# Performance work log

Hardware: AMD Instinct MI355X
Metric: run time of the kernel (lower is better)

The kernel has to match this reference:

```python
import jax, jax.numpy as jnp
import numpy as np

NUM_FEATURE = 512
HIDDEN = 256
NUM_CLASSES = 10
L1 = 1e-4
ALPHA = 1e-3
BATCH = 65536


def setup_inputs() -> dict:
    key = jax.random.key(0)
    k = jax.random.split(key, 6)
    x = jax.random.normal(k[0], (BATCH, NUM_FEATURE), dtype=jnp.float32)
    y = jax.random.randint(k[1], (BATCH,), 0, NUM_CLASSES, dtype=jnp.int32)
    fc0 = jax.random.normal(k[2], (NUM_FEATURE, 512), dtype=jnp.float32) / NUM_FEATURE
    fc1 = jax.random.normal(k[3], (NUM_FEATURE, 512), dtype=jnp.float32) / NUM_FEATURE
    w = jax.random.normal(k[4], (NUM_FEATURE, HIDDEN), dtype=jnp.float32) / NUM_FEATURE
    w1 = jax.random.normal(k[5], (HIDDEN, NUM_CLASSES), dtype=jnp.float32) / HIDDEN
    return {"x": x, "y": y, "fc0": fc0, "fc1": fc1, "w": w, "w1": w1}


def reference(x, y, fc0, fc1, w, w1):
    # sigmoid-gated MLP block with residual
    x1 = x @ fc0                                   # [B, 512]
    x2 = jax.nn.relu(x @ fc1)                      # [B, 512]
    x4 = x + (1.0 + jax.nn.sigmoid(x1)) * x2       # [B, 512] residual

    # head (Dropout(p=0.0) is identity)
    logits = jax.nn.relu(x4 @ w) @ w1              # [B, 10]
    pred = jnp.argmax(logits, axis=1)

    # cross-entropy (mean over batch)
    logp = jax.nn.log_softmax(logits, axis=-1)
    ce = -jnp.mean(jnp.take_along_axis(logp, y[:, None].astype(jnp.int32), axis=1))

    # L1 penalty on all weight matrices
    l1_pen = L1 * (jnp.abs(w1).sum() + jnp.abs(w).sum()
                   + jnp.abs(fc0).sum() + jnp.abs(fc1).sum())

    # per-class variance: sum_i ||mean_{y_i} - x4_i||^2, vectorized via segment sums
    counts = jax.ops.segment_sum(jnp.ones((x4.shape[0],), jnp.float32), y,
                                 num_segments=NUM_CLASSES)
    sums = jax.ops.segment_sum(x4, y, num_segments=NUM_CLASSES)   # [10, 512]
    means = sums / jnp.maximum(counts, 1.0)[:, None]
    var_loss = jnp.sum(jnp.square(means[y] - x4))

    loss = ce + l1_pen + ALPHA * var_loss
    acc = jnp.mean((pred.astype(jnp.int32) == y.astype(jnp.int32)).astype(jnp.float32))
    return (loss, acc)
```

## Files before the change

kernel.cpp:

```cpp
#include <hip/hip_runtime.h>
#include <stdint.h>

#define BATCH 65536
#define FDIM 512
#define HDIM 256
#define NC 10
#define NREP 16

typedef short short8 __attribute__((ext_vector_type(8)));
typedef float f32x4 __attribute__((ext_vector_type(4)));

#define OFF_FC0T   ((size_t)0)
#define OFF_FC1T   (OFF_FC0T + (size_t)512*512*2)
#define OFF_WT     (OFF_FC1T + (size_t)512*512*2)
#define OFF_XT     (OFF_WT   + (size_t)256*512*2)
#define OFF_X4T    (OFF_XT   + (size_t)BATCH*512*2)
#define OFF_ACC    (OFF_X4T  + (size_t)BATCH*512*2)
#define SCAL_SUMSQ 0
#define SCAL_CE    16
#define SCAL_ACC   32
#define SCAL_L1    48
#define SCAL_CTR   64
#define SCAL_N     128
#define CNT_OFF    SCAL_N
#define GSUM_OFF   (SCAL_N + NREP*16)
#define ACC_FLOATS (GSUM_OFF + NREP*5120)
#define OFF_W1T    (OFF_ACC + (size_t)ACC_FLOATS*4)

#define GLL(g,l) __builtin_amdgcn_global_load_lds((const __attribute__((address_space(1))) void*)(g), (__attribute__((address_space(3))) void*)(l), 16, 0, 0)

__device__ __forceinline__ unsigned short f2b(float f){
  unsigned u = __float_as_uint(f);
  u += 0x7FFFu + ((u >> 16) & 1u);
  return (unsigned short)(u >> 16);
}
__device__ __forceinline__ float b2f(unsigned short h){
  return __uint_as_float(((unsigned)h) << 16);
}
__device__ __forceinline__ unsigned pk2b(float f0, float f1){
  unsigned u0 = __float_as_uint(f0) + 0x8000u;
  unsigned u1 = __float_as_uint(f1) + 0x8000u;
  return __builtin_amdgcn_perm(u1, u0, 0x07060302u);
}
__device__ __forceinline__ float ald(const float* p){
  return __hip_atomic_load(p, __ATOMIC_RELAXED, __HIP_MEMORY_SCOPE_AGENT);
}

__global__ __launch_bounds__(256) void k_setup(
    const float* __restrict__ x,   const float* __restrict__ fc0,
    const float* __restrict__ fc1, const float* __restrict__ w,
    const float* __restrict__ w1,  const int* __restrict__ y,
    unsigned short* __restrict__ xT,   unsigned short* __restrict__ fc0T,
    unsigned short* __restrict__ fc1T, unsigned short* __restrict__ wT,
    unsigned short* __restrict__ w1T,  float* __restrict__ accb)
{
  int blk = blockIdx.x, t = threadIdx.x;
  if (blk < 2048){
    __shared__ __align__(16) unsigned short xls[16*520];
    int wv = t >> 6, l = t & 63;
    #pragma unroll 1
    for (int it = 0; it < 2; ++it){
      int I = blk*2 + it;
      #pragma unroll
      for (int rr = 0; rr < 4; ++rr){
        int row = wv*4 + rr;
        const float* src = x + ((size_t)(I*16 + row))*FDIM + l*8;
        float4 v0 = *(const float4*)src;
        float4 v1 = *(const float4*)(src + 4);
        unsigned o[4];
        o[0] = pk2b(v0.x, v0.y); o[1] = pk2b(v0.z, v0.w);
        o[2] = pk2b(v1.x, v1.y); o[3] = pk2b(v1.z, v1.w);
        *(short8*)&xls[row*520 + l*8] = *(short8*)o;
      }
      __syncthreads();
      #pragma unroll
      for (int cc = 0; cc < 4; ++cc){
        int C = cc*4 + wv;
        short8 v = *(const short8*)&xls[(l & 15)*520 + C*32 + (l >> 4)*8];
        *(short8*)&xT[(((size_t)I*16 + C) << 9) + l*8] = v;
      }
      __syncthreads();
    }
    return;
  }
  if (blk < 2384){
    int i = (blk - 2048)*256 + t;
    float l1v = 0.f;
    if (i < 32768){
      int n4 = i&15, m = (i>>4)&3, C = (i>>6)&15, J = i>>10;
      int n = J*16+n4, k8 = C*4+m;
      unsigned short o[8];
      #pragma unroll
      for (int j=0;j<8;++j){ float v = fc0[(size_t)(k8*8+j)*512 + n]; o[j]=f2b(v); l1v += fabsf(v); }
      *(short8*)&fc0T[(size_t)(J*16+C)*512 + (i&63)*8] = *(short8*)o;
    } else if (i < 65536){
      int j0 = i - 32768;
      int n4 = j0&15, m = (j0>>4)&3, C = (j0>>6)&15, J = j0>>10;
      int n = J*16+n4, k8 = C*4+m;
      unsigned short o[8];
      #pragma unroll
      for (int j=0;j<8;++j){ float v = fc1[(size_t)(k8*8+j)*512 + n]; o[j]=f2b(v); l1v += fabsf(v); }
      *(short8*)&fc1T[(size_t)(J*16+C)*512 + (j0&63)*8] = *(short8*)o;
    } else if (i < 81920){
      int j0 = i - 65536;
      int n4 = j0&15, m = (j0>>4)&3, C = (j0>>6)&15, J = j0>>10;
      int n = J*16+n4, k8 = C*4+m;
      unsigned short o[8];
      #pragma unroll
      for (int j=0;j<8;++j){ float v = w[(size_t)(k8*8+j)*256 + n]; o[j]=f2b(v); l1v += fabsf(v); }
      *(short8*)&wT[(size_t)(J*16+C)*512 + (j0&63)*8] = *(short8*)o;
    } else if (i < 86016){
      int j0 = i - 81920;
      int C = j0 >> 9, l = (j0 >> 3) & 63, e = j0 & 7;
      int n = l & 15, k = C*32 + (l>>4)*8 + e;
      float v = (n < NC) ? w1[k*NC + n] : 0.f;
      w1T[C*512 + l*8 + e] = f2b(v);
      if (n < NC) l1v = fabsf(v);
    }
    for (int off = 32; off; off >>= 1) l1v += __shfl_down(l1v, off);
    if ((t & 63) == 0 && l1v != 0.f)
      atomicAdd(&accb[SCAL_L1 + (blk & (NREP-1))], l1v);
    return;
  }
  if (blk < 2465){
    int base = (blk - 2384)*1024;
    #pragma unroll
    for (int j=0;j<4;++j){
      int idx = base + j*256 + t;
      if (idx < ACC_FLOATS && (idx < CNT_OFF || idx >= CNT_OFF + NREP*16))
        accb[idx] = 0.f;
    }
    return;
  }
  {
    __shared__ float cntS[16];
    int b = blk - 2465;
    if (t < 16) cntS[t] = 0.f;
    __syncthreads();
    int base = b*4096;
    for (int i = t; i < 4096; i += 256) atomicAdd(&cntS[y[base+i]], 1.f);
    __syncthreads();
    if (t < 16) accb[CNT_OFF + b*16 + t] = cntS[t];
  }
}


#define BARRIER() __builtin_amdgcn_s_barrier()
#define LGKM0() do{ asm volatile("s_waitcnt lgkmcnt(0)" ::: "memory"); \
                    __builtin_amdgcn_sched_barrier(0); }while(0)

#define RA(AB, C) do{                                                         \
  _Pragma("unroll") for (int m_=0;m_<8;++m_)                                  \
    a[m_] = *(const short8*)((AB) + (((wr*8+m_)*2 + (C))<<10) + lane*16);     \
}while(0)

#define RB(AB, MAT, C) do{                                                    \
  _Pragma("unroll") for (int n_=0;n_<2;++n_)                                  \
    bb[n_] = *(const short8*)((AB) + 32768 + (MAT)*16384 +                    \
                              (((wc*2+n_)*2 + (C))<<10) + lane*16);           \
}while(0)

#define MM16(ACC) do{                                                         \
  __builtin_amdgcn_s_setprio(1);                                              \
  _Pragma("unroll") for (int n_=0;n_<2;++n_)                                  \
  _Pragma("unroll") for (int m_=0;m_<8;++m_)                                  \
    ACC[m_][n_] = __builtin_amdgcn_mfma_f32_16x16x32_bf16(a[m_], bb[n_], ACC[m_][n_], 0,0,0); \
  __builtin_amdgcn_s_setprio(0);                                              \
}while(0)

#define SA(KT, C) do{                                                         \
  char* d_ = ldsd + (((KT)&1) ? 65536 : 0);                                   \
  _Pragma("unroll") for (int r_=0;r_<2;++r_){                                 \
    int I_ = wv + r_*8;                                                       \
    GLL(xb + (((size_t)((rowblk*16 + I_)*16 + (KT)*2 + (C))) << 10) + lane*16,\
        d_ + ((I_*2 + (C)) << 10) + lane*16);                                 \
  } }while(0)

#define SB(KT, C) do{                                                         \
  char* d_ = ldsd + (((KT)&1) ? 65536 : 0) + 32768;                           \
  GLL(b0b + (((size_t)((colblk*8 + wv)*16 + (KT)*2 + (C))) << 10) + lane*16,  \
      d_ + ((wv*2 + (C)) << 10) + lane*16);                                   \
  GLL(b1b + (((size_t)((colblk*8 + wv)*16 + (KT)*2 + (C))) << 10) + lane*16,  \
      d_ + 16384 + ((wv*2 + (C)) << 10) + lane*16);                           \
}while(0)

#define KLOOP() do{                                                           \
  SA(0,0); SB(0,0); SA(0,1); SB(0,1); SA(1,0); SB(1,0); SA(1,1);              \
  asm volatile("s_waitcnt vmcnt(6)" ::: "memory");                            \
  __builtin_amdgcn_sched_barrier(0);                                          \
  BARRIER();                                                                  \
  _Pragma("unroll")                                                           \
  for (int i = 0; i < 4; ++i){                                                \
    int kt0 = 2*i, kt1 = 2*i+1;                                               \
    char* Ab0 = ldsd + ((kt0 & 1) ? 65536 : 0);                               \
    char* Ab1 = ldsd + ((kt1 & 1) ? 65536 : 0);                               \
    RA(Ab0, 0); RB(Ab0, 0, 0);                                                \
    SB(kt1, 1);                                                               \
    BARRIER(); LGKM0(); MM16(acc1);                                           \
    BARRIER();                                                                \
    RB(Ab0, 1, 0);                                                            \
    if (i < 3) SA(kt0+2, 0);                                                  \
    BARRIER(); LGKM0(); MM16(acc2);                                           \
    BARRIER();                                                                \
    RA(Ab0, 1); RB(Ab0, 0, 1);                                                \
    if (i < 3) SB(kt0+2, 0);                                                  \
    BARRIER(); LGKM0(); MM16(acc1);                                           \
    BARRIER();                                                                \
    RB(Ab0, 1, 1);                                                            \
    if (i < 3) SA(kt0+2, 1);                                                  \
    BARRIER(); LGKM0(); MM16(acc2);                                           \
    if (i < 3) { asm volatile("s_waitcnt vmcnt(6)" ::: "memory"); }           \
    else       { asm volatile("s_waitcnt vmcnt(0)" ::: "memory"); }           \
    __builtin_amdgcn_sched_barrier(0);                                        \
    BARRIER();                                                                \
    RA(Ab1, 0); RB(Ab1, 0, 0);                                                \
    if (i < 3) SB(kt0+2, 1);                                                  \
    BARRIER(); LGKM0(); MM16(acc1);                                           \
    BARRIER();                                                                \
    RB(Ab1, 1, 0);                                                            \
    if (i < 3) SA(kt1+2, 0);                                                  \
    BARRIER(); LGKM0(); MM16(acc2);                                           \
    BARRIER();                                                                \
    RA(Ab1, 1); RB(Ab1, 0, 1);                                                \
    if (i < 3) SB(kt1+2, 0);                                                  \
    BARRIER(); LGKM0(); MM16(acc1);                                           \
    BARRIER();                                                                \
    RB(Ab1, 1, 1);                                                            \
    if (i < 3) SA(kt1+2, 1);                                                  \
    BARRIER(); LGKM0(); MM16(acc2);                                           \
    if (i < 3) { asm volatile("s_waitcnt vmcnt(6)" ::: "memory");             \
                 __builtin_amdgcn_sched_barrier(0); }                         \
    BARRIER();                                                                \
  }                                                                           \
}while(0)

__global__ __launch_bounds__(512, 2) void k_gemm12(
    const unsigned short* __restrict__ xT,
    const unsigned short* __restrict__ fc0T,
    const unsigned short* __restrict__ fc1T,
    const int* __restrict__ y,
    unsigned short* __restrict__ x4T,
    float* __restrict__ accb)
{
  extern __shared__ __align__(16) char ldsd[];
  float* scal = accb;
  float* gsum = accb + GSUM_OFF;

  int blk = blockIdx.x;
  int wg = (blk & 7)*128 + (blk >> 3);
  int rowblk = wg >> 2;
  int colblk = wg & 3;

  int t = threadIdx.x;
  int wv = t >> 6, lane = t & 63, ln = lane & 15, quad = lane >> 4;
  int wr = wv >> 2, wc = wv & 3;

  const char* xb  = (const char*)xT;
  const char* b0b = (const char*)fc0T;
  const char* b1b = (const char*)fc1T;

  const f32x4 zv = {0.f,0.f,0.f,0.f};
  f32x4 acc1[8][2], acc2[8][2];
  #pragma unroll
  for (int m=0;m<8;++m){ acc1[m][0]=zv; acc1[m][1]=zv; acc2[m][0]=zv; acc2[m][1]=zv; }

  short8 a[8], bb[2];

  KLOOP();

  {
    int Cres = colblk*4 + wc;
    #pragma unroll
    for (int i = 0; i < 8; ++i){
      GLL(xb + (((size_t)((rowblk*16 + wr*8 + i)*16 + Cres)) << 10) + lane*16,
          ldsd + ((wv*8 + i) << 10) + lane*16);
    }
    asm volatile("s_waitcnt vmcnt(0)" ::: "memory");
  }
  __syncthreads();

  unsigned short* resU = (unsigned short*)ldsd;
  unsigned short* x4U  = (unsigned short*)(ldsd + 65536);
  float sumsq = 0.f;
  #pragma unroll
  for (int m = 0; m < 8; ++m){
    #pragma unroll
    for (int n = 0; n < 2; ++n){
      #pragma unroll
      for (int r = 0; r < 4; ++r){
        int slot = (quad*4 + r) | ((n*2 + (ln>>3)) << 4);
        int idx = ((wv*8 + m) << 9) + slot*8 + (ln & 7);
        float xv  = b2f(resU[idx]);
        float x1v = acc1[m][n][r];
        float x2v = fmaxf(acc2[m][n][r], 0.f);
        float gate = 1.f + 1.f/(1.f + __expf(-x1v));
        float x4v = fmaf(gate, x2v, xv);
        unsigned short ub = f2b(x4v);
        float fq = b2f(ub);
        sumsq = fmaf(fq, fq, sumsq);
        x4U[idx] = ub;
        acc1[m][n][r] = fq;
      }
    }
  }
  for (int off = 32; off; off >>= 1) sumsq += __shfl_down(sumsq, off);
  __syncthreads();

  float cs[NC][2];
  #pragma unroll
  for (int c=0;c<NC;++c){ cs[c][0]=0.f; cs[c][1]=0.f; }
  {
    const int* yrow = y + rowblk*256 + wr*128;
    #pragma unroll
    for (int m = 0; m < 8; ++m){
      int yv[4];
      #pragma unroll
      for (int r = 0; r < 4; ++r) yv[r] = yrow[m*16 + quad*4 + r];
      #pragma unroll
      for (int r = 0; r < 4; ++r){
        float v0 = acc1[m][0][r], v1 = acc1[m][1][r];
        #pragma unroll
        for (int c = 0; c < NC; ++c){
          bool msk = (yv[r] == c);
          cs[c][0] += msk ? v0 : 0.f;
          cs[c][1] += msk ? v1 : 0.f;
        }
      }
    }
  }
  #pragma unroll
  for (int c = 0; c < NC; ++c)
    #pragma unroll
    for (int n = 0; n < 2; ++n){
      cs[c][n] += __shfl_xor(cs[c][n], 16);
      cs[c][n] += __shfl_xor(cs[c][n], 32);
    }

  float* red = (float*)ldsd;
  float* ct  = (float*)(ldsd + 4096);
  if (lane == 0) red[wv] = sumsq;
  if (lane < 16){
    #pragma unroll
    for (int c = 0; c < NC; ++c)
      #pragma unroll
      for (int n = 0; n < 2; ++n)
        ct[((wv*NC + c)*2 + n)*16 + ln] = cs[c][n];
  }
  __syncthreads();
  if (t == 0){
    float s = 0.f;
    #pragma unroll
    for (int i=0;i<8;++i) s += red[i];
    atomicAdd(&scal[SCAL_SUMSQ + (blk & (NREP-1))], s);
  }
  #pragma unroll
  for (int r = 0; r < 2; ++r){
    int o = r*512 + t;
    int tile = o >> 6, off16 = o & 63;
    int wvp = tile >> 3, i = tile & 7;
    size_t Ig = (size_t)rowblk*16 + (wvp>>2)*8 + i;
    int Cg = colblk*4 + (wvp & 3);
    *(short8*)&x4T[((Ig*16 + Cg) << 9) + off16*8] =
      *(const short8*)&x4U[(tile << 9) + off16*8];
  }
  for (int i = t; i < NC*128; i += 512){
    int c = i >> 7, col = i & 127;
    int wcx = col >> 5, nx = (col >> 4) & 1, lnx = col & 15;
    float v = ct[((wcx*NC + c)*2 + nx)*16 + lnx]
            + ct[(((4+wcx)*NC + c)*2 + nx)*16 + lnx];
    atomicAdd(&gsum[(size_t)(blk & (NREP-1))*5120 + c*512 + colblk*128 + col], v);
  }
}

__global__ __launch_bounds__(512, 2) void k_gemm3_head(
    const unsigned short* __restrict__ x4T,
    const unsigned short* __restrict__ wT,
    const unsigned short* __restrict__ w1T,
    const int* __restrict__ y,
    float* __restrict__ accb,
    float* __restrict__ out)
{
  extern __shared__ __align__(16) char ldsd[];
  __shared__ float redc[8], reda[8];
  __shared__ int lastB;

  float* scal = accb;

  int blk = blockIdx.x;
  int rowblk = blk;
  const int colblk = 0;

  int t = threadIdx.x;
  int wv = t >> 6, lane = t & 63, ln = lane & 15, quad = lane >> 4;
  int wr = wv >> 2, wc = wv & 3;
  int rep = (blk ^ (blk >> 4)) & (NREP-1);

  const char* xb  = (const char*)x4T;
  const char* b0b = (const char*)wT;
  const char* b1b = (const char*)wT + (size_t)128*1024;

  const f32x4 zv = {0.f,0.f,0.f,0.f};
  f32x4 acc1[8][2], acc2[8][2];
  #pragma unroll
  for (int m=0;m<8;++m){ acc1[m][0]=zv; acc1[m][1]=zv; acc2[m][0]=zv; acc2[m][1]=zv; }

  short8 a[8], bb[2];

  KLOOP();

  short8 bw1[8];
  #pragma unroll
  for (int Ck = 0; Ck < 8; ++Ck)
    bw1[Ck] = *(const short8*)&w1T[Ck*512 + lane*8];

  unsigned short* transH = (unsigned short*)ldsd;
  #pragma unroll
  for (int m = 0; m < 8; ++m){
    #pragma unroll
    for (int n = 0; n < 2; ++n){
      #pragma unroll
      for (int r = 0; r < 4; ++r){
        int slot = (quad*4 + r) | ((n*2 + (ln>>3)) << 4);
        int e = ln & 7;
        int IhA = wr*8 + m;
        transH[((IhA*8 + wc)     << 9) + slot*8 + e] = f2b(fmaxf(acc1[m][n][r], 0.f));
        transH[((IhA*8 + 4 + wc) << 9) + slot*8 + e] = f2b(fmaxf(acc2[m][n][r], 0.f));
      }
    }
  }
  __syncthreads();

  f32x4 alog[2] = {zv, zv};
  #pragma unroll
  for (int ih = 0; ih < 2; ++ih){
    int Ih = wv*2 + ih;
    #pragma unroll
    for (int Ck = 0; Ck < 8; ++Ck){
      short8 af = *(const short8*)&transH[((Ih*8 + Ck) << 9) + lane*8];
      alog[ih] = __builtin_amdgcn_mfma_f32_16x16x32_bf16(af, bw1[Ck], alog[ih], 0,0,0);
    }
  }

  float ce_l = 0.f, acc_l = 0.f;
  #pragma unroll
  for (int ih = 0; ih < 2; ++ih){
    #pragma unroll
    for (int r = 0; r < 4; ++r){
      int grow = blk*256 + (wv*2 + ih)*16 + quad*4 + r;
      int yv = y[grow];
      float lg = (ln < NC) ? alog[ih][r] : -1e30f;
      float m = lg; int mi = ln;
      #pragma unroll
      for (int mk = 1; mk < 16; mk <<= 1){
        float om = __shfl_xor(m, mk); int oi = __shfl_xor(mi, mk);
        if (om > m || (om == m && oi < mi)){ m = om; mi = oi; }
      }
      float e  = (ln < NC) ? __expf(lg - m) : 0.f;
      float sy = (ln == yv) ? lg : 0.f;
      #pragma unroll
      for (int mk = 1; mk < 16; mk <<= 1){ e += __shfl_xor(e, mk); sy += __shfl_xor(sy, mk); }
      float lse = m + __logf(e);
      if (ln == 0){ ce_l += (lse - sy); acc_l += (mi == yv) ? 1.f : 0.f; }
    }
  }
  ce_l  += __shfl_down(ce_l, 16);  acc_l += __shfl_down(acc_l, 16);
  ce_l  += __shfl_down(ce_l, 32);  acc_l += __shfl_down(acc_l, 32);
  if (lane == 0){ redc[wv] = ce_l; reda[wv] = acc_l; }
  __syncthreads();
  if (t == 0){
    float c = 0.f, aa = 0.f;
    #pragma unroll
    for (int i=0;i<8;++i){ c += redc[i]; aa += reda[i]; }
    atomicAdd(&scal[SCAL_CE  + rep], c);
    atomicAdd(&scal[SCAL_ACC + rep], aa);
    __threadfence();
    int prev = atomicAdd((int*)(scal + SCAL_CTR), 1);
    lastB = (prev == (int)gridDim.x - 1);
  }
  __syncthreads();
  if (!lastB) return;

  {
    const float* gsum = accb + GSUM_OFF;
    const float* gcnt = accb + CNT_OFF;
    float contrib = 0.f;
    for (int idx = t; idx < 5120; idx += 512){
      float S = 0.f;
      #pragma unroll
      for (int r = 0; r < NREP; ++r) S += ald(&gsum[(size_t)r*5120 + idx]);
      int c = idx >> 9;
      float cnt = 0.f;
      #pragma unroll
      for (int r = 0; r < NREP; ++r) cnt += ald(&gcnt[r*16 + c]);
      contrib += S*S / fmaxf(cnt, 1.f);
    }
    for (int off = 32; off; off >>= 1) contrib += __shfl_down(contrib, off);
    __syncthreads();
    if (lane == 0) redc[wv] = contrib;
    __syncthreads();
    if (t == 0){
      float var2 = 0.f;
      #pragma unroll
      for (int i=0;i<8;++i) var2 += redc[i];
      float sumsq=0.f, ce=0.f, accv=0.f, l1=0.f;
      for (int r=0;r<NREP;++r){
        sumsq += ald(&scal[SCAL_SUMSQ+r]);
        ce    += ald(&scal[SCAL_CE+r]);
        accv  += ald(&scal[SCAL_ACC+r]);
        l1    += ald(&scal[SCAL_L1+r]);
      }
      float var_loss = sumsq - var2;
      out[0] = ce/(float)BATCH + 1e-4f*l1 + 1e-3f*var_loss;
      out[1] = accv/(float)BATCH;
    }
  }
}

extern "C" void kernel_launch(void* const* d_in, const int* in_sizes, int n_in,
                              void* d_out, int out_size, void* d_ws, size_t ws_size,
                              hipStream_t stream){
  (void)in_sizes; (void)n_in; (void)out_size; (void)ws_size;
  const float* x   = (const float*)d_in[0];
  const int*   y   = (const int*)d_in[1];
  const float* fc0 = (const float*)d_in[2];
  const float* fc1 = (const float*)d_in[3];
  const float* w   = (const float*)d_in[4];
  const float* w1  = (const float*)d_in[5];
  char* ws = (char*)d_ws;
  unsigned short* fc0T = (unsigned short*)(ws + OFF_FC0T);
  unsigned short* fc1T = (unsigned short*)(ws + OFF_FC1T);
  unsigned short* wT   = (unsigned short*)(ws + OFF_WT);
  unsigned short* xT   = (unsigned short*)(ws + OFF_XT);
  unsigned short* x4T  = (unsigned short*)(ws + OFF_X4T);
  unsigned short* w1T  = (unsigned short*)(ws + OFF_W1T);
  float* accb = (float*)(ws + OFF_ACC);

  static bool once = [](){
    hipFuncSetAttribute((const void*)k_gemm12,
                        hipFuncAttributeMaxDynamicSharedMemorySize, 131072);
    hipFuncSetAttribute((const void*)k_gemm3_head,
                        hipFuncAttributeMaxDynamicSharedMemorySize, 131072);
    return true;
  }();
  (void)once;

  k_setup<<<2481, 256, 0, stream>>>(x, fc0, fc1, w, w1, y, xT, fc0T, fc1T, wT, w1T, accb);
  k_gemm12<<<1024, 512, 131072, stream>>>(xT, fc0T, fc1T, y, x4T, accb);
  k_gemm3_head<<<256, 512, 131072, stream>>>(x4T, wT, w1T, y, accb, (float*)d_out);
}
```

Before: 354.8 us.

## Fuse setup and both GEMM stages into one persistent cooperative kernel

Replaces the three launches (setup, gemm12, gemm3+head) with one cooperative kernel of 256 blocks that uses grid.sync between phases. Each block now loops over four column tiles of the first GEMM instead of using 1024 separate blocks, and y labels are staged in LDS. The aim is to remove launch gaps and the last-block atomic counter. In exchange, occupancy drops to one 512-thread block per CU, 256 blocks cover 256 CUs, and grid-wide barriers add their own cost.

```diff
diff --git a/kernel.cpp b/kernel.cpp
--- a/kernel.cpp
+++ b/kernel.cpp
@@ -1,5 +1,8 @@
 #include <hip/hip_runtime.h>
+#include <hip/hip_cooperative_groups.h>
 #include <stdint.h>
+
+namespace cg = cooperative_groups;
 
 #define BATCH 65536
 #define FDIM 512
@@ -20,7 +23,6 @@
 #define SCAL_CE    16
 #define SCAL_ACC   32
 #define SCAL_L1    48
-#define SCAL_CTR   64
 #define SCAL_N     128
 #define CNT_OFF    SCAL_N
 #define GSUM_OFF   (SCAL_N + NREP*16)
@@ -46,104 +48,6 @@
   return __hip_atomic_load(p, __ATOMIC_RELAXED, __HIP_MEMORY_SCOPE_AGENT);
 }
 
-__global__ __launch_bounds__(256) void k_setup(
-    const float* __restrict__ x,   const float* __restrict__ fc0,
-    const float* __restrict__ fc1, const float* __restrict__ w,
-    const float* __restrict__ w1,  const int* __restrict__ y,
-    unsigned short* __restrict__ xT,   unsigned short* __restrict__ fc0T,
-    unsigned short* __restrict__ fc1T, unsigned short* __restrict__ wT,
-    unsigned short* __restrict__ w1T,  float* __restrict__ accb)
-{
-  int blk = blockIdx.x, t = threadIdx.x;
-  if (blk < 2048){
-    __shared__ __align__(16) unsigned short xls[16*520];
-    int wv = t >> 6, l = t & 63;
-    #pragma unroll 1
-    for (int it = 0; it < 2; ++it){
-      int I = blk*2 + it;
-      #pragma unroll
-      for (int rr = 0; rr < 4; ++rr){
-        int row = wv*4 + rr;
-        const float* src = x + ((size_t)(I*16 + row))*FDIM + l*8;
-        float4 v0 = *(const float4*)src;
-        float4 v1 = *(const float4*)(src + 4);
-        unsigned o[4];
-        o[0] = pk2b(v0.x, v0.y); o[1] = pk2b(v0.z, v0.w);
-        o[2] = pk2b(v1.x, v1.y); o[3] = pk2b(v1.z, v1.w);
-        *(short8*)&xls[row*520 + l*8] = *(short8*)o;
-      }
-      __syncthreads();
-      #pragma unroll
-      for (int cc = 0; cc < 4; ++cc){
-        int C = cc*4 + wv;
-        short8 v = *(const short8*)&xls[(l & 15)*520 + C*32 + (l >> 4)*8];
-        *(short8*)&xT[(((size_t)I*16 + C) << 9) + l*8] = v;
-      }
-      __syncthreads();
-    }
-    return;
-  }
-  if (blk < 2384){
-    int i = (blk - 2048)*256 + t;
-    float l1v = 0.f;
-    if (i < 32768){
-      int n4 = i&15, m = (i>>4)&3, C = (i>>6)&15, J = i>>10;
-      int n = J*16+n4, k8 = C*4+m;
-      unsigned short o[8];
-      #pragma unroll
-      for (int j=0;j<8;++j){ float v = fc0[(size_t)(k8*8+j)*512 + n]; o[j]=f2b(v); l1v += fabsf(v); }
-      *(short8*)&fc0T[(size_t)(J*16+C)*512 + (i&63)*8] = *(short8*)o;
-    } else if (i < 65536){
-      int j0 = i - 32768;
-      int n4 = j0&15, m = (j0>>4)&3, C = (j0>>6)&15, J = j0>>10;
-      int n = J*16+n4, k8 = C*4+m;
-      unsigned short o[8];
-      #pragma unroll
-      for (int j=0;j<8;++j){ float v = fc1[(size_t)(k8*8+j)*512 + n]; o[j]=f2b(v); l1v += fabsf(v); }
-      *(short8*)&fc1T[(size_t)(J*16+C)*512 + (j0&63)*8] = *(short8*)o;
-    } else if (i < 81920){
-      int j0 = i - 65536;
-      int n4 = j0&15, m = (j0>>4)&3, C = (j0>>6)&15, J = j0>>10;
-      int n = J*16+n4, k8 = C*4+m;
-      unsigned short o[8];
-      #pragma unroll
-      for (int j=0;j<8;++j){ float v = w[(size_t)(k8*8+j)*256 + n]; o[j]=f2b(v); l1v += fabsf(v); }
-      *(short8*)&wT[(size_t)(J*16+C)*512 + (j0&63)*8] = *(short8*)o;
-    } else if (i < 86016){
-      int j0 = i - 81920;
-      int C = j0 >> 9, l = (j0 >> 3) & 63, e = j0 & 7;
-      int n = l & 15, k = C*32 + (l>>4)*8 + e;
-      float v = (n < NC) ? w1[k*NC + n] : 0.f;
-      w1T[C*512 + l*8 + e] = f2b(v);
-      if (n < NC) l1v = fabsf(v);
-    }
-    for (int off = 32; off; off >>= 1) l1v += __shfl_down(l1v, off);
-    if ((t & 63) == 0 && l1v != 0.f)
-      atomicAdd(&accb[SCAL_L1 + (blk & (NREP-1))], l1v);
-    return;
-  }
-  if (blk < 2465){
-    int base = (blk - 2384)*1024;
-    #pragma unroll
-    for (int j=0;j<4;++j){
-      int idx = base + j*256 + t;
-      if (idx < ACC_FLOATS && (idx < CNT_OFF || idx >= CNT_OFF + NREP*16))
-        accb[idx] = 0.f;
-    }
-    return;
-  }
-  {
-    __shared__ float cntS[16];
-    int b = blk - 2465;
-    if (t < 16) cntS[t] = 0.f;
-    __syncthreads();
-    int base = b*4096;
-    for (int i = t; i < 4096; i += 256) atomicAdd(&cntS[y[base+i]], 1.f);
-    __syncthreads();
-    if (t < 16) accb[CNT_OFF + b*16 + t] = cntS[t];
-  }
-}
-
 
 #define BARRIER() __builtin_amdgcn_s_barrier()
 #define LGKM0() do{ asm volatile("s_waitcnt lgkmcnt(0)" ::: "memory"); \
@@ -234,254 +138,318 @@
   }                                                                           \
 }while(0)
 
-__global__ __launch_bounds__(512, 2) void k_gemm12(
-    const unsigned short* __restrict__ xT,
-    const unsigned short* __restrict__ fc0T,
-    const unsigned short* __restrict__ fc1T,
-    const int* __restrict__ y,
-    unsigned short* __restrict__ x4T,
-    float* __restrict__ accb)
-{
-  extern __shared__ __align__(16) char ldsd[];
-  float* scal = accb;
-  float* gsum = accb + GSUM_OFF;
-
-  int blk = blockIdx.x;
-  int wg = (blk & 7)*128 + (blk >> 3);
-  int rowblk = wg >> 2;
-  int colblk = wg & 3;
-
-  int t = threadIdx.x;
-  int wv = t >> 6, lane = t & 63, ln = lane & 15, quad = lane >> 4;
-  int wr = wv >> 2, wc = wv & 3;
-
-  const char* xb  = (const char*)xT;
-  const char* b0b = (const char*)fc0T;
-  const char* b1b = (const char*)fc1T;
-
-  const f32x4 zv = {0.f,0.f,0.f,0.f};
-  f32x4 acc1[8][2], acc2[8][2];
-  #pragma unroll
-  for (int m=0;m<8;++m){ acc1[m][0]=zv; acc1[m][1]=zv; acc2[m][0]=zv; acc2[m][1]=zv; }
-
-  short8 a[8], bb[2];
-
-  KLOOP();
-
-  {
-    int Cres = colblk*4 + wc;
-    #pragma unroll
-    for (int i = 0; i < 8; ++i){
-      GLL(xb + (((size_t)((rowblk*16 + wr*8 + i)*16 + Cres)) << 10) + lane*16,
-          ldsd + ((wv*8 + i) << 10) + lane*16);
-    }
-    asm volatile("s_waitcnt vmcnt(0)" ::: "memory");
-  }
-  __syncthreads();
-
-  unsigned short* resU = (unsigned short*)ldsd;
-  unsigned short* x4U  = (unsigned short*)(ldsd + 65536);
-  float sumsq = 0.f;
-  #pragma unroll
-  for (int m = 0; m < 8; ++m){
-    #pragma unroll
-    for (int n = 0; n < 2; ++n){
-      #pragma unroll
-      for (int r = 0; r < 4; ++r){
-        int slot = (quad*4 + r) | ((n*2 + (ln>>3)) << 4);
-        int idx = ((wv*8 + m) << 9) + slot*8 + (ln & 7);
-        float xv  = b2f(resU[idx]);
-        float x1v = acc1[m][n][r];
-        float x2v = fmaxf(acc2[m][n][r], 0.f);
-        float gate = 1.f + 1.f/(1.f + __expf(-x1v));
-        float x4v = fmaf(gate, x2v, xv);
-        unsigned short ub = f2b(x4v);
-        float fq = b2f(ub);
-        sumsq = fmaf(fq, fq, sumsq);
-        x4U[idx] = ub;
-        acc1[m][n][r] = fq;
-      }
-    }
-  }
-  for (int off = 32; off; off >>= 1) sumsq += __shfl_down(sumsq, off);
-  __syncthreads();
-
-  float cs[NC][2];
-  #pragma unroll
-  for (int c=0;c<NC;++c){ cs[c][0]=0.f; cs[c][1]=0.f; }
-  {
-    const int* yrow = y + rowblk*256 + wr*128;
-    #pragma unroll
-    for (int m = 0; m < 8; ++m){
-      int yv[4];
-      #pragma unroll
-      for (int r = 0; r < 4; ++r) yv[r] = yrow[m*16 + quad*4 + r];
-      #pragma unroll
-      for (int r = 0; r < 4; ++r){
-        float v0 = acc1[m][0][r], v1 = acc1[m][1][r];
-        #pragma unroll
-        for (int c = 0; c < NC; ++c){
-          bool msk = (yv[r] == c);
-          cs[c][0] += msk ? v0 : 0.f;
-          cs[c][1] += msk ? v1 : 0.f;
-        }
-      }
-    }
-  }
-  #pragma unroll
-  for (int c = 0; c < NC; ++c)
-    #pragma unroll
-    for (int n = 0; n < 2; ++n){
-      cs[c][n] += __shfl_xor(cs[c][n], 16);
-      cs[c][n] += __shfl_xor(cs[c][n], 32);
-    }
-
-  float* red = (float*)ldsd;
-  float* ct  = (float*)(ldsd + 4096);
-  if (lane == 0) red[wv] = sumsq;
-  if (lane < 16){
-    #pragma unroll
-    for (int c = 0; c < NC; ++c)
-      #pragma unroll
-      for (int n = 0; n < 2; ++n)
-        ct[((wv*NC + c)*2 + n)*16 + ln] = cs[c][n];
-  }
-  __syncthreads();
-  if (t == 0){
-    float s = 0.f;
-    #pragma unroll
-    for (int i=0;i<8;++i) s += red[i];
-    atomicAdd(&scal[SCAL_SUMSQ + (blk & (NREP-1))], s);
-  }
-  #pragma unroll
-  for (int r = 0; r < 2; ++r){
-    int o = r*512 + t;
-    int tile = o >> 6, off16 = o & 63;
-    int wvp = tile >> 3, i = tile & 7;
-    size_t Ig = (size_t)rowblk*16 + (wvp>>2)*8 + i;
-    int Cg = colblk*4 + (wvp & 3);
-    *(short8*)&x4T[((Ig*16 + Cg) << 9) + off16*8] =
-      *(const short8*)&x4U[(tile << 9) + off16*8];
-  }
-  for (int i = t; i < NC*128; i += 512){
-    int c = i >> 7, col = i & 127;
-    int wcx = col >> 5, nx = (col >> 4) & 1, lnx = col & 15;
-    float v = ct[((wcx*NC + c)*2 + nx)*16 + lnx]
-            + ct[(((4+wcx)*NC + c)*2 + nx)*16 + lnx];
-    atomicAdd(&gsum[(size_t)(blk & (NREP-1))*5120 + c*512 + colblk*128 + col], v);
-  }
-}
-
-__global__ __launch_bounds__(512, 2) void k_gemm3_head(
-    const unsigned short* __restrict__ x4T,
-    const unsigned short* __restrict__ wT,
-    const unsigned short* __restrict__ w1T,
-    const int* __restrict__ y,
-    float* __restrict__ accb,
-    float* __restrict__ out)
+__global__ __launch_bounds__(512, 1) void k_fused(
+    const float* __restrict__ x,   const int* __restrict__ y,
+    const float* __restrict__ fc0, const float* __restrict__ fc1,
+    const float* __restrict__ w,   const float* __restrict__ w1,
+    unsigned short* __restrict__ xT,   unsigned short* __restrict__ fc0T,
+    unsigned short* __restrict__ fc1T, unsigned short* __restrict__ wT,
+    unsigned short* __restrict__ w1T,  unsigned short* __restrict__ x4T,
+    float* __restrict__ accb,          float* __restrict__ out)
 {
   extern __shared__ __align__(16) char ldsd[];
   __shared__ float redc[8], reda[8];
-  __shared__ int lastB;
-
-  float* scal = accb;
-
-  int blk = blockIdx.x;
-  int rowblk = blk;
-  const int colblk = 0;
-
-  int t = threadIdx.x;
+  cg::grid_group grid = cg::this_grid();
+
+  int blk = blockIdx.x, t = threadIdx.x;
   int wv = t >> 6, lane = t & 63, ln = lane & 15, quad = lane >> 4;
   int wr = wv >> 2, wc = wv & 3;
-  int rep = (blk ^ (blk >> 4)) & (NREP-1);
-
-  const char* xb  = (const char*)x4T;
-  const char* b0b = (const char*)wT;
-  const char* b1b = (const char*)wT + (size_t)128*1024;
-
-  const f32x4 zv = {0.f,0.f,0.f,0.f};
-  f32x4 acc1[8][2], acc2[8][2];
-  #pragma unroll
-  for (int m=0;m<8;++m){ acc1[m][0]=zv; acc1[m][1]=zv; acc2[m][0]=zv; acc2[m][1]=zv; }
-
-  short8 a[8], bb[2];
-
-  KLOOP();
-
-  short8 bw1[8];
-  #pragma unroll
-  for (int Ck = 0; Ck < 8; ++Ck)
-    bw1[Ck] = *(const short8*)&w1T[Ck*512 + lane*8];
-
-  unsigned short* transH = (unsigned short*)ldsd;
-  #pragma unroll
-  for (int m = 0; m < 8; ++m){
+
+  float* scal = accb;
+  float* gsum = accb + GSUM_OFF;
+
+  if (blk >= 240){
+    float* cntS = (float*)ldsd;
+    if (t < 16) cntS[t] = 0.f;
+    __syncthreads();
+    int base = (blk - 240)*4096;
+    for (int i = t; i < 4096; i += 512) atomicAdd(&cntS[y[base+i]], 1.f);
+    __syncthreads();
+    if (t < 16) accb[CNT_OFF + (blk - 240)*16 + t] = cntS[t];
+    __syncthreads();
+  }
+  if (blk < 168){
+    int i = blk*512 + t;
+    float l1v = 0.f;
+    if (i < 32768){
+      int n4 = i&15, m = (i>>4)&3, C = (i>>6)&15, J = i>>10;
+      int n = J*16+n4, k8 = C*4+m;
+      unsigned short o[8];
+      #pragma unroll
+      for (int j=0;j<8;++j){ float v = fc0[(size_t)(k8*8+j)*512 + n]; o[j]=f2b(v); l1v += fabsf(v); }
+      *(short8*)&fc0T[(size_t)(J*16+C)*512 + (i&63)*8] = *(short8*)o;
+    } else if (i < 65536){
+      int j0 = i - 32768;
+      int n4 = j0&15, m = (j0>>4)&3, C = (j0>>6)&15, J = j0>>10;
+      int n = J*16+n4, k8 = C*4+m;
+      unsigned short o[8];
+      #pragma unroll
+      for (int j=0;j<8;++j){ float v = fc1[(size_t)(k8*8+j)*512 + n]; o[j]=f2b(v); l1v += fabsf(v); }
+      *(short8*)&fc1T[(size_t)(J*16+C)*512 + (j0&63)*8] = *(short8*)o;
+    } else if (i < 81920){
+      int j0 = i - 65536;
+      int n4 = j0&15, m = (j0>>4)&3, C = (j0>>6)&15, J = j0>>10;
+      int n = J*16+n4, k8 = C*4+m;
+      unsigned short o[8];
+      #pragma unroll
+      for (int j=0;j<8;++j){ float v = w[(size_t)(k8*8+j)*256 + n]; o[j]=f2b(v); l1v += fabsf(v); }
+      *(short8*)&wT[(size_t)(J*16+C)*512 + (j0&63)*8] = *(short8*)o;
+    } else {
+      int j0 = i - 81920;
+      int C = j0 >> 9, l = (j0 >> 3) & 63, e = j0 & 7;
+      int n = l & 15, k = C*32 + (l>>4)*8 + e;
+      float v = (n < NC) ? w1[k*NC + n] : 0.f;
+      w1T[C*512 + l*8 + e] = f2b(v);
+      if (n < NC) l1v = fabsf(v);
+    }
+    for (int off = 32; off; off >>= 1) l1v += __shfl_down(l1v, off);
+    if ((t & 63) == 0 && l1v != 0.f)
+      atomicAdd(&accb[SCAL_L1 + (blk & (NREP-1))], l1v);
+  }
+  if (blk >= 88 && blk < 249){
+    int idx = (blk - 88)*512 + t;
+    if (idx < ACC_FLOATS && (idx < CNT_OFF || idx >= CNT_OFF + NREP*16))
+      accb[idx] = 0.f;
+  }
+  {
+    int g = wv >> 2, wv4 = wv & 3;
+    unsigned short* xls = (unsigned short*)(ldsd + g*17408);
+    #pragma unroll 1
+    for (int it = 0; it < 8; ++it){
+      int I = blk*16 + it*2 + g;
+      #pragma unroll
+      for (int rr = 0; rr < 4; ++rr){
+        int row = wv4*4 + rr;
+        const float* src = x + ((size_t)(I*16 + row))*FDIM + lane*8;
+        float4 v0 = *(const float4*)src;
+        float4 v1 = *(const float4*)(src + 4);
+        unsigned o[4];
+        o[0] = pk2b(v0.x, v0.y); o[1] = pk2b(v0.z, v0.w);
+        o[2] = pk2b(v1.x, v1.y); o[3] = pk2b(v1.z, v1.w);
+        *(short8*)&xls[row*520 + lane*8] = *(short8*)o;
+      }
+      __syncthreads();
+      #pragma unroll
+      for (int cc = 0; cc < 4; ++cc){
+        int C = cc*4 + wv4;
+        short8 v = *(const short8*)&xls[(lane & 15)*520 + C*32 + (lane >> 4)*8];
+        *(short8*)&xT[(((size_t)I*16 + C) << 9) + lane*8] = v;
+      }
+      __syncthreads();
+    }
+  }
+  grid.sync();
+
+  {
+    const char* xb  = (const char*)xT;
+    const char* b0b = (const char*)fc0T;
+    const char* b1b = (const char*)fc1T;
+    int rowblk = blk;
+    #pragma unroll 1
+    for (int cb = 0; cb < 4; ++cb){
+      int colblk = cb;
+      const f32x4 zv = {0.f,0.f,0.f,0.f};
+      f32x4 acc1[8][2], acc2[8][2];
+      #pragma unroll
+      for (int m=0;m<8;++m){ acc1[m][0]=zv; acc1[m][1]=zv; acc2[m][0]=zv; acc2[m][1]=zv; }
+      short8 a[8], bb[2];
+
+      KLOOP();
+
+      {
+        int Cres = colblk*4 + wc;
+        #pragma unroll
+        for (int i = 0; i < 8; ++i){
+          GLL(xb + (((size_t)((rowblk*16 + wr*8 + i)*16 + Cres)) << 10) + lane*16,
+              ldsd + ((wv*8 + i) << 10) + lane*16);
+        }
+        asm volatile("s_waitcnt vmcnt(0)" ::: "memory");
+      }
+      __syncthreads();
+
+      unsigned short* resU = (unsigned short*)ldsd;
+      unsigned short* x4U  = (unsigned short*)(ldsd + 65536);
+      float sumsq = 0.f;
+      #pragma unroll
+      for (int m = 0; m < 8; ++m){
+        #pragma unroll
+        for (int n = 0; n < 2; ++n){
+          #pragma unroll
+          for (int r = 0; r < 4; ++r){
+            int slot = (quad*4 + r) | ((n*2 + (ln>>3)) << 4);
+            int idx = ((wv*8 + m) << 9) + slot*8 + (ln & 7);
+            float xv  = b2f(resU[idx]);
+            float x1v = acc1[m][n][r];
+            float x2v = fmaxf(acc2[m][n][r], 0.f);
+            float gate = 1.f + 1.f/(1.f + __expf(-x1v));
+            float x4v = fmaf(gate, x2v, xv);
+            unsigned short ub = f2b(x4v);
+            float fq = b2f(ub);
+            sumsq = fmaf(fq, fq, sumsq);
+            x4U[idx] = ub;
+            acc1[m][n][r] = fq;
+          }
+        }
+      }
+      for (int off = 32; off; off >>= 1) sumsq += __shfl_down(sumsq, off);
+      __syncthreads();
+
+      float* red = (float*)ldsd;
+      int*   yS  = (int*)(ldsd + 64);
+      float* ct  = (float*)(ldsd + 2048);
+      if (t < 256) yS[t] = y[rowblk*256 + t];
+      if (lane == 0) red[wv] = sumsq;
+      __syncthreads();
+
+      float cs[NC][2];
+      #pragma unroll
+      for (int c=0;c<NC;++c){ cs[c][0]=0.f; cs[c][1]=0.f; }
+      {
+        const int* yrow = yS + wr*128;
+        #pragma unroll
+        for (int m = 0; m < 8; ++m){
+          #pragma unroll
+          for (int r = 0; r < 4; ++r){
+            int yv = yrow[m*16 + quad*4 + r];
+            float v0 = acc1[m][0][r], v1 = acc1[m][1][r];
+            #pragma unroll
+            for (int c = 0; c < NC; ++c){
+              bool msk = (yv == c);
+              cs[c][0] += msk ? v0 : 0.f;
+              cs[c][1] += msk ? v1 : 0.f;
+            }
+          }
+        }
+      }
+      #pragma unroll
+      for (int c = 0; c < NC; ++c)
+        #pragma unroll
+        for (int n = 0; n < 2; ++n){
+          cs[c][n] += __shfl_xor(cs[c][n], 16);
+          cs[c][n] += __shfl_xor(cs[c][n], 32);
+        }
+      if (lane < 16){
+        #pragma unroll
+        for (int c = 0; c < NC; ++c)
+          #pragma unroll
+          for (int n = 0; n < 2; ++n)
+            ct[((wv*NC + c)*2 + n)*16 + ln] = cs[c][n];
+      }
+      __syncthreads();
+      if (t == 0){
+        float s = 0.f;
+        #pragma unroll
+        for (int i=0;i<8;++i) s += red[i];
+        atomicAdd(&scal[SCAL_SUMSQ + (blk & (NREP-1))], s);
+      }
+      #pragma unroll
+      for (int r = 0; r < 2; ++r){
+        int o = r*512 + t;
+        int tile = o >> 6, off16 = o & 63;
+        int wvp = tile >> 3, i = tile & 7;
+        size_t Ig = (size_t)rowblk*16 + (wvp>>2)*8 + i;
+        int Cg = colblk*4 + (wvp & 3);
+        *(short8*)&x4T[((Ig*16 + Cg) << 9) + off16*8] =
+          *(const short8*)&x4U[(tile << 9) + off16*8];
+      }
+      for (int i = t; i < NC*128; i += 512){
+        int c = i >> 7, col = i & 127;
+        int wcx = col >> 5, nx = (col >> 4) & 1, lnx = col & 15;
+        float v = ct[((wcx*NC + c)*2 + nx)*16 + lnx]
+                + ct[(((4+wcx)*NC + c)*2 + nx)*16 + lnx];
+        atomicAdd(&gsum[(size_t)(blk & (NREP-1))*5120 + c*512 + colblk*128 + col], v);
+      }
+      __syncthreads();
+    }
+  }
+  grid.sync();
+
+  {
+    const char* xb  = (const char*)x4T;
+    const char* b0b = (const char*)wT;
+    const char* b1b = (const char*)wT + (size_t)128*1024;
+    int rowblk = blk;
+    const int colblk = 0;
+    int rep = (blk ^ (blk >> 4)) & (NREP-1);
+
+    const f32x4 zv = {0.f,0.f,0.f,0.f};
+    f32x4 acc1[8][2], acc2[8][2];
     #pragma unroll
-    for (int n = 0; n < 2; ++n){
+    for (int m=0;m<8;++m){ acc1[m][0]=zv; acc1[m][1]=zv; acc2[m][0]=zv; acc2[m][1]=zv; }
+    short8 a[8], bb[2];
+
+    KLOOP();
+
+    short8 bw1[8];
+    #pragma unroll
+    for (int Ck = 0; Ck < 8; ++Ck)
+      bw1[Ck] = *(const short8*)&w1T[Ck*512 + lane*8];
+
+    unsigned short* transH = (unsigned short*)ldsd;
+    #pragma unroll
+    for (int m = 0; m < 8; ++m){
+      #pragma unroll
+      for (int n = 0; n < 2; ++n){
+        #pragma unroll
+        for (int r = 0; r < 4; ++r){
+          int slot = (quad*4 + r) | ((n*2 + (ln>>3)) << 4);
+          int e = ln & 7;
+          int IhA = wr*8 + m;
+          transH[((IhA*8 + wc)     << 9) + slot*8 + e] = f2b(fmaxf(acc1[m][n][r], 0.f));
+          transH[((IhA*8 + 4 + wc) << 9) + slot*8 + e] = f2b(fmaxf(acc2[m][n][r], 0.f));
+        }
+      }
+    }
+    __syncthreads();
+
+    f32x4 alog[2] = {zv, zv};
+    #pragma unroll
+    for (int ih = 0; ih < 2; ++ih){
+      int Ih = wv*2 + ih;
+      #pragma unroll
+      for (int Ck = 0; Ck < 8; ++Ck){
+        short8 af = *(const short8*)&transH[((Ih*8 + Ck) << 9) + lane*8];
+        alog[ih] = __builtin_amdgcn_mfma_f32_16x16x32_bf16(af, bw1[Ck], alog[ih], 0,0,0);
+      }
+    }
+
+    float ce_l = 0.f, acc_l = 0.f;
+    #pragma unroll
+    for (int ih = 0; ih < 2; ++ih){
       #pragma unroll
       for (int r = 0; r < 4; ++r){
-        int slot = (quad*4 + r) | ((n*2 + (ln>>3)) << 4);
-        int e = ln & 7;
-        int IhA = wr*8 + m;
-        transH[((IhA*8 + wc)     << 9) + slot*8 + e] = f2b(fmaxf(acc1[m][n][r], 0.f));
-        transH[((IhA*8 + 4 + wc) << 9) + slot*8 + e] = f2b(fmaxf(acc2[m][n][r], 0.f));
-      }
-    }
-  }
-  __syncthreads();
-
-  f32x4 alog[2] = {zv, zv};
-  #pragma unroll
-  for (int ih = 0; ih < 2; ++ih){
-    int Ih = wv*2 + ih;
-    #pragma unroll
-    for (int Ck = 0; Ck < 8; ++Ck){
-      short8 af = *(const short8*)&transH[((Ih*8 + Ck) << 9) + lane*8];
-      alog[ih] = __builtin_amdgcn_mfma_f32_16x16x32_bf16(af, bw1[Ck], alog[ih], 0,0,0);
-    }
-  }
-
-  float ce_l = 0.f, acc_l = 0.f;
-  #pragma unroll
-  for (int ih = 0; ih < 2; ++ih){
-    #pragma unroll
-    for (int r = 0; r < 4; ++r){
-      int grow = blk*256 + (wv*2 + ih)*16 + quad*4 + r;
-      int yv = y[grow];
-      float lg = (ln < NC) ? alog[ih][r] : -1e30f;
-      float m = lg; int mi = ln;
-      #pragma unroll
-      for (int mk = 1; mk < 16; mk <<= 1){
-        float om = __shfl_xor(m, mk); int oi = __shfl_xor(mi, mk);
-        if (om > m || (om == m && oi < mi)){ m = om; mi = oi; }
-      }
-      float e  = (ln < NC) ? __expf(lg - m) : 0.f;
-      float sy = (ln == yv) ? lg : 0.f;
-      #pragma unroll
-      for (int mk = 1; mk < 16; mk <<= 1){ e += __shfl_xor(e, mk); sy += __shfl_xor(sy, mk); }
-      float lse = m + __logf(e);
-      if (ln == 0){ ce_l += (lse - sy); acc_l += (mi == yv) ? 1.f : 0.f; }
-    }
-  }
-  ce_l  += __shfl_down(ce_l, 16);  acc_l += __shfl_down(acc_l, 16);
-  ce_l  += __shfl_down(ce_l, 32);  acc_l += __shfl_down(acc_l, 32);
-  if (lane == 0){ redc[wv] = ce_l; reda[wv] = acc_l; }
-  __syncthreads();
-  if (t == 0){
-    float c = 0.f, aa = 0.f;
-    #pragma unroll
-    for (int i=0;i<8;++i){ c += redc[i]; aa += reda[i]; }
-    atomicAdd(&scal[SCAL_CE  + rep], c);
-    atomicAdd(&scal[SCAL_ACC + rep], aa);
-    __threadfence();
-    int prev = atomicAdd((int*)(scal + SCAL_CTR), 1);
-    lastB = (prev == (int)gridDim.x - 1);
-  }
-  __syncthreads();
-  if (!lastB) return;
-
-  {
-    const float* gsum = accb + GSUM_OFF;
+        int grow = blk*256 + (wv*2 + ih)*16 + quad*4 + r;
+        int yv = y[grow];
+        float lg = (ln < NC) ? alog[ih][r] : -1e30f;
+        float m = lg; int mi = ln;
+        #pragma unroll
+        for (int mk = 1; mk < 16; mk <<= 1){
+          float om = __shfl_xor(m, mk); int oi = __shfl_xor(mi, mk);
+          if (om > m || (om == m && oi < mi)){ m = om; mi = oi; }
+        }
+        float e  = (ln < NC) ? __expf(lg - m) : 0.f;
+        float sy = (ln == yv) ? lg : 0.f;
+        #pragma unroll
+        for (int mk = 1; mk < 16; mk <<= 1){ e += __shfl_xor(e, mk); sy += __shfl_xor(sy, mk); }
+        float lse = m + __logf(e);
+        if (ln == 0){ ce_l += (lse - sy); acc_l += (mi == yv) ? 1.f : 0.f; }
+      }
+    }
+    ce_l  += __shfl_down(ce_l, 16);  acc_l += __shfl_down(acc_l, 16);
+    ce_l  += __shfl_down(ce_l, 32);  acc_l += __shfl_down(acc_l, 32);
+    if (lane == 0){ redc[wv] = ce_l; reda[wv] = acc_l; }
+    __syncthreads();
+    if (t == 0){
+      float c = 0.f, aa = 0.f;
+      #pragma unroll
+      for (int i=0;i<8;++i){ c += redc[i]; aa += reda[i]; }
+      atomicAdd(&scal[SCAL_CE  + rep], c);
+      atomicAdd(&scal[SCAL_ACC + rep], aa);
+    }
+  }
+  grid.sync();
+
+  if (blk == 0){
     const float* gcnt = accb + CNT_OFF;
     float contrib = 0.f;
     for (int idx = t; idx < 5120; idx += 512){
@@ -534,17 +502,20 @@
   unsigned short* x4T  = (unsigned short*)(ws + OFF_X4T);
   unsigned short* w1T  = (unsigned short*)(ws + OFF_W1T);
   float* accb = (float*)(ws + OFF_ACC);
+  float* out  = (float*)d_out;
 
   static bool once = [](){
-    hipFuncSetAttribute((const void*)k_gemm12,
-                        hipFuncAttributeMaxDynamicSharedMemorySize, 131072);
-    hipFuncSetAttribute((const void*)k_gemm3_head,
+    hipFuncSetAttribute((const void*)k_fused,
                         hipFuncAttributeMaxDynamicSharedMemorySize, 131072);
     return true;
   }();
   (void)once;
 
-  k_setup<<<2481, 256, 0, stream>>>(x, fc0, fc1, w, w1, y, xT, fc0T, fc1T, wT, w1T, accb);
-  k_gemm12<<<1024, 512, 131072, stream>>>(xT, fc0T, fc1T, y, x4T, accb);
-  k_gemm3_head<<<256, 512, 131072, stream>>>(x4T, wT, w1T, y, accb, (float*)d_out);
+  void* kargs[] = {
+    (void*)&x, (void*)&y, (void*)&fc0, (void*)&fc1, (void*)&w, (void*)&w1,
+    (void*)&xT, (void*)&fc0T, (void*)&fc1T, (void*)&wT, (void*)&w1T,
+    (void*)&x4T, (void*)&accb, (void*)&out
+  };
+  hipLaunchCooperativeKernel((const void*)k_fused, dim3(256), dim3(512),
+                             kargs, 131072, stream);
 }
```

Result: slower. 650.3 us (+83.3%).
